# Kernel optimization log

Hardware: AMD Instinct MI355X
Metric: run time of the kernel (lower is better)

## Reference

```python
import jax, jax.numpy as jnp
import numpy as np

K = 8192      # num_embeddings
D = 512       # embedding_dim
DECAY = 0.99
EPS = 1e-5


def setup_inputs() -> dict:
    key = jax.random.key(0)
    k1, k2, k3 = jax.random.split(key, 3)
    inputs = jax.random.normal(k1, (8, 2048, D), dtype=jnp.float32)
    weight = jax.random.normal(k2, (K, D), dtype=jnp.float32) * 0.01
    ema_cluster_size = jnp.ones((K,), dtype=jnp.float32)
    ema_w = jax.random.normal(k3, (K, D), dtype=jnp.float32) * 0.01
    return {"inputs": inputs, "weight": weight,
            "ema_cluster_size": ema_cluster_size, "ema_w": ema_w}


def _l2norm(x):
    return x / jnp.sqrt(jnp.sum(x * x, axis=-1, keepdims=True) + 1e-12)


def reference(inputs, weight, ema_cluster_size, ema_w):
    # Flatten tokens: [N, D]
    flat = inputs.reshape(-1, D)
    cb = _l2norm(weight)            # [K, D]
    xn = _l2norm(flat)              # [N, D]
    # distances = 2 - 2 * sim; argmin(dist) == argmax(sim)
    sim = jnp.einsum('nd,kd->nk', xn, cb)          # [N, K]
    idx = jnp.argmax(sim, axis=1)                  # [N]
    # quantized = one_hot(idx) @ weight  ==  gather
    quantized = weight[idx].reshape(inputs.shape)
    # EMA codebook update (training path)
    counts = jax.ops.segment_sum(jnp.ones_like(idx, dtype=inputs.dtype), idx,
                                 num_segments=K)   # one_hot.sum(0)
    new_cs = ema_cluster_size * DECAY + (1.0 - DECAY) * counts
    n = jnp.sum(new_cs)
    new_cs = (new_cs + EPS) / (n + K * EPS) * n
    dw = jax.ops.segment_sum(flat, idx, num_segments=K)  # one_hot.T @ flat
    new_ema_w = ema_w * DECAY + (1.0 - DECAY) * dw
    new_weight = new_ema_w / new_cs[:, None]
    # Commitment loss and straight-through estimator
    e_latent_loss = jnp.mean((jax.lax.stop_gradient(quantized) - inputs) ** 2)
    quantized_st = inputs + jax.lax.stop_gradient(quantized - inputs)
    return (quantized_st, e_latent_loss, idx[:, None],
            new_cs, new_ema_w, new_weight)
```

## Files before the change

kernel.cpp:

```cpp
#include <hip/hip_runtime.h>
#include <cstdint>
#include <cstddef>

#define NTOK 16384
#define DIM  512
#define KCB  8192
#define MARGIN 6.0e-3f
#define LISTCAP 512

typedef short s16x8 __attribute__((ext_vector_type(8)));
typedef float f32x4 __attribute__((ext_vector_type(4)));

static const size_t WS_XN   = 0;
static const size_t WS_WN   = 16777216;
static const size_t WS_KV   = 25165824;
static const size_t WS_LP   = 37748736;
static const size_t WS_N    = 37847040;
static const size_t WS_CNT  = 37847296;
static const size_t WS_LIST = 37880064;

__device__ __forceinline__ void gl_lds16(const void* g, void* l) {
  __builtin_amdgcn_global_load_lds(
      (__attribute__((address_space(1))) void*)(uintptr_t)g,
      (__attribute__((address_space(3))) void*)(uint32_t)(uintptr_t)l,
      16, 0, 0);
}

__device__ __forceinline__ unsigned short f2bf(float f) {
  unsigned int u = __float_as_uint(f);
  u = (u + 0x7fffu + ((u >> 16) & 1u)) >> 16;
  return (unsigned short)u;
}

__global__ __launch_bounds__(256) void k_normalize(const float* __restrict__ x,
                                                   const float* __restrict__ w,
                                                   unsigned short* __restrict__ xn,
                                                   unsigned short* __restrict__ wn) {
  const int row = blockIdx.x;
  const int tid = threadIdx.x, lane = tid & 63, wave = tid >> 6;
  const float* src;
  unsigned short* dst;
  if (row < NTOK) { src = x + (size_t)row * DIM;          dst = xn + (size_t)row * DIM; }
  else            { src = w + (size_t)(row - NTOK) * DIM; dst = wn + (size_t)(row - NTOK) * DIM; }
  const int e = tid * 2;
  float2 v = *(const float2*)(src + e);
  float ss = v.x * v.x + v.y * v.y;
  #pragma unroll
  for (int off = 32; off > 0; off >>= 1) ss += __shfl_xor(ss, off);
  __shared__ float red[4];
  if (lane == 0) red[wave] = ss;
  __syncthreads();
  const float s = red[0] + red[1] + red[2] + red[3];
  const float inv = rsqrtf(s + 1e-12f);
  unsigned int lo = f2bf(v.x * inv), hi = f2bf(v.y * inv);
  *(unsigned int*)(dst + e) = lo | (hi << 16);
}

__global__ __launch_bounds__(256, 2) void k_gemm_top2(const unsigned short* __restrict__ xn,
                                                      const unsigned short* __restrict__ wn,
                                                      uint2* __restrict__ kv) {
  __shared__ __align__(16) unsigned short smA[128 * 64];
  __shared__ __align__(16) unsigned short smB[256 * 64];
  const int tid = threadIdx.x, wave = tid >> 6, lane = tid & 63;
  const int quad = lane >> 4, col = lane & 15;
  const int wave_m = (wave & 1) * 64, wave_n = (wave >> 1) * 128;
  const int n0 = blockIdx.x * 256, m0 = blockIdx.y * 128;

  const unsigned short* pA[4];
  const unsigned short* pB[8];
  unsigned short* dA[4];
  unsigned short* dB[8];
  #pragma unroll
  for (int i = 0; i < 4; ++i) {
    int s = wave * 256 + i * 64 + lane;
    int row = s >> 3, cg = (s & 7) ^ (row & 7);
    pA[i] = xn + (size_t)(m0 + row) * DIM + cg * 8;
    dA[i] = &smA[(size_t)(wave * 256 + i * 64) * 8];
  }
  #pragma unroll
  for (int i = 0; i < 8; ++i) {
    int s = wave * 512 + i * 64 + lane;
    int row = s >> 3, cg = (s & 7) ^ (row & 7);
    pB[i] = wn + (size_t)(n0 + row) * DIM + cg * 8;
    dB[i] = &smB[(size_t)(wave * 512 + i * 64) * 8];
  }

  int offA[4][2], offB[8][2];
  #pragma unroll
  for (int kbi = 0; kbi < 2; ++kbi) {
    int kb = kbi * 4 + quad;
    #pragma unroll
    for (int mi = 0; mi < 4; ++mi) {
      int row = wave_m + mi * 16 + col;
      offA[mi][kbi] = (row * 8 + (kb ^ (row & 7))) * 16;
    }
    #pragma unroll
    for (int ni = 0; ni < 8; ++ni) {
      int row = wave_n + ni * 16 + col;
      offB[ni][kbi] = (row * 8 + (kb ^ (row & 7))) * 16;
    }
  }

  f32x4 acc[4][8] = {};
  const char* sA = (const char*)smA;
  const char* sB = (const char*)smB;

  #pragma unroll 1
  for (int kt = 0; kt < 8; ++kt) {
    __syncthreads();
    #pragma unroll
    for (int i = 0; i < 4; ++i) { gl_lds16(pA[i], dA[i]); pA[i] += 64; }
    #pragma unroll
    for (int i = 0; i < 8; ++i) { gl_lds16(pB[i], dB[i]); pB[i] += 64; }
    __syncthreads();
    #pragma unroll
    for (int kbi = 0; kbi < 2; ++kbi) {
      s16x8 af[4], bfr[8];
      #pragma unroll
      for (int mi = 0; mi < 4; ++mi) af[mi]  = *(const s16x8*)(sA + offA[mi][kbi]);
      #pragma unroll
      for (int ni = 0; ni < 8; ++ni) bfr[ni] = *(const s16x8*)(sB + offB[ni][kbi]);
      #pragma unroll
      for (int mi = 0; mi < 4; ++mi)
        #pragma unroll
        for (int ni = 0; ni < 8; ++ni)
          acc[mi][ni] = __builtin_amdgcn_mfma_f32_16x16x32_bf16(af[mi], bfr[ni], acc[mi][ni], 0, 0, 0);
    }
  }

  const int tile = blockIdx.x * 2 + (wave >> 1);
  unsigned int rk1 = 0, rk2 = 0;
  #pragma unroll
  for (int mi = 0; mi < 4; ++mi) {
    #pragma unroll
    for (int r = 0; r < 4; ++r) {
      const int p = mi * 4 + r;
      unsigned int k1 = 0, k2 = 0;
      #pragma unroll
      for (int ni = 0; ni < 8; ++ni) {
        float vb = acc[mi][ni][r] + 2.0f;
        unsigned int key = (__float_as_uint(vb) & ~0x7Fu) | (unsigned int)(ni * 16 + col);
        unsigned int mn = min(k1, key);
        k1 = max(k1, key);
        k2 = max(k2, mn);
      }
      #pragma unroll
      for (int off = 1; off < 16; off <<= 1) {
        unsigned int o1 = (unsigned int)__shfl_xor((int)k1, off);
        unsigned int o2 = (unsigned int)__shfl_xor((int)k2, off);
        unsigned int mn = min(k1, o1);
        k1 = max(k1, o1);
        k2 = max(max(k2, o2), mn);
      }
      if (col == p) { rk1 = k1; rk2 = k2; }
    }
  }
  const int row = wave_m + (col >> 2) * 16 + quad * 4 + (col & 3);
  kv[(size_t)(m0 + row) * 64 + tile] = make_uint2(rk1, rk2);
}

__global__ __launch_bounds__(256) void k_select(const float* __restrict__ x,
                                                const float* __restrict__ wgt,
                                                const uint2* __restrict__ kv,
                                                float* __restrict__ out0,
                                                float* __restrict__ out_idx,
                                                float* __restrict__ lp,
                                                int* __restrict__ cnt,
                                                int* __restrict__ list) {
  const int wave = threadIdx.x >> 6, lane = threadIdx.x & 63;
  const int t = blockIdx.x * 4 + wave;

  const uint2 kp = kv[(size_t)t * 64 + lane];
  const float v1 = __uint_as_float(kp.x);
  const float v2 = __uint_as_float(kp.y);
  const int   i1 = lane * 128 + (int)(kp.x & 0x7Fu);

  float gm = v1;
  #pragma unroll
  for (int off = 32; off > 0; off >>= 1) gm = fmaxf(gm, __shfl_xor(gm, off));
  const float thresh = gm - MARGIN;

  unsigned long long m1 = __ballot(v1 >= thresh);
  unsigned long long m2 = __ballot(v2 >= thresh);

  const float* xrow = x + (size_t)t * DIM;
  const float* xr = xrow + lane * 8;
  float4 x0 = *(const float4*)xr;
  float4 x1 = *(const float4*)(xr + 4);
  double xv[8] = {x0.x, x0.y, x0.z, x0.w, x1.x, x1.y, x1.z, x1.w};

  int besti;
  if (__popcll(m1) == 1 && m2 == 0ull) {
    besti = __shfl(i1, __builtin_ctzll(m1));
  } else {
    double bestv = -1e300; besti = 1 << 30;

    auto evalc = [&](int c) {
      const float* wr = wgt + (size_t)c * DIM + lane * 8;
      float4 w0 = *(const float4*)wr;
      float4 w1 = *(const float4*)(wr + 4);
      double s  = (double)w0.x * xv[0] + (double)w0.y * xv[1] + (double)w0.z * xv[2] + (double)w0.w * xv[3]
                + (double)w1.x * xv[4] + (double)w1.y * xv[5] + (double)w1.z * xv[6] + (double)w1.w * xv[7];
      double nw = (double)w0.x * w0.x + (double)w0.y * w0.y + (double)w0.z * w0.z + (double)w0.w * w0.w
                + (double)w1.x * w1.x + (double)w1.y * w1.y + (double)w1.z * w1.z + (double)w1.w * w1.w;
      #pragma unroll
      for (int off = 1; off < 64; off <<= 1) { s += __shfl_xor(s, off); nw += __shfl_xor(nw, off); }
      double sim = s / sqrt(nw + 1e-12);
      if (sim > bestv || (sim == bestv && c < besti)) { bestv = sim; besti = c; }
    };

    unsigned long long w1m = m1;
    while (w1m) {
      int b = __builtin_ctzll(w1m); w1m &= w1m - 1;
      evalc(__shfl(i1, b));
    }
    unsigned long long w2m = m2;
    while (w2m) {
      int b = __builtin_ctzll(w2m); w2m &= w2m - 1;
      #pragma unroll 1
      for (int chunk = 0; chunk < 2; ++chunk) {
        const int c = b * 128 + chunk * 64 + lane;
        const float* wr = wgt + (size_t)c * DIM;
        double s = 0.0, nw = 0.0;
        #pragma unroll 4
        for (int d = 0; d < DIM; d += 4) {
          float4 wv = *(const float4*)(wr + d);
          float4 xw = *(const float4*)(xrow + d);
          s  += (double)wv.x * xw.x + (double)wv.y * xw.y + (double)wv.z * xw.z + (double)wv.w * xw.w;
          nw += (double)wv.x * wv.x + (double)wv.y * wv.y + (double)wv.z * wv.z + (double)wv.w * wv.w;
        }
        double sim = s / sqrt(nw + 1e-12);
        if (sim > bestv || (sim == bestv && c < besti)) { bestv = sim; besti = c; }
      }
    }
    #pragma unroll
    for (int off = 1; off < 64; off <<= 1) {
      double ov = __shfl_xor(bestv, off);
      int    oi = __shfl_xor(besti, off);
      if (ov > bestv || (ov == bestv && oi < besti)) { bestv = ov; besti = oi; }
    }
  }
  if ((unsigned)besti >= KCB) besti = 0;

  const float* wr = wgt + (size_t)besti * DIM + lane * 8;
  float4 w0 = *(const float4*)wr;
  float4 w1 = *(const float4*)(wr + 4);
  float* o0 = out0 + (size_t)t * DIM + lane * 8;
  *(float4*)o0 = w0;
  *(float4*)(o0 + 4) = w1;
  double d2 = 0.0;
  double qv[8] = {w0.x, w0.y, w0.z, w0.w, w1.x, w1.y, w1.z, w1.w};
  #pragma unroll
  for (int j = 0; j < 8; ++j) { double d = qv[j] - xv[j]; d2 += d * d; }
  #pragma unroll
  for (int off = 1; off < 64; off <<= 1) d2 += __shfl_xor(d2, off);

  if (lane == 0) {
    lp[t] = (float)d2;
    out_idx[t] = (float)besti;
    int slot = atomicAdd(&cnt[besti], 1);
    if (slot < LISTCAP) list[besti * LISTCAP + slot] = t;
  }
}

__global__ __launch_bounds__(256) void k_scalars(const float* __restrict__ cs,
                                                 const float* __restrict__ lp,
                                                 double* __restrict__ nacc,
                                                 double* __restrict__ lacc) {
  const int tid = threadIdx.x, b = blockIdx.x;
  const int wave = tid >> 6, lane = tid & 63;
  double s = (double)cs[b * 256 + tid];
  float2 l2 = *(const float2*)(lp + b * 512 + tid * 2);
  double l = (double)l2.x + (double)l2.y;
  #pragma unroll
  for (int off = 32; off > 0; off >>= 1) { s += __shfl_xor(s, off); l += __shfl_xor(l, off); }
  __shared__ double rs[4], rl[4];
  if (lane == 0) { rs[wave] = s; rl[wave] = l; }
  __syncthreads();
  if (tid == 0) {
    atomicAdd(nacc, 0.99 * (rs[0] + rs[1] + rs[2] + rs[3]));
    atomicAdd(lacc, rl[0] + rl[1] + rl[2] + rl[3]);
  }
}

__global__ __launch_bounds__(256) void k_dw(const float* __restrict__ x,
                                            const float* __restrict__ ema_w,
                                            const float* __restrict__ cs,
                                            const int* __restrict__ cnt,
                                            const int* __restrict__ list,
                                            const double* __restrict__ nacc,
                                            const double* __restrict__ lacc,
                                            float* __restrict__ out1,
                                            float* __restrict__ out3,
                                            float* __restrict__ out4,
                                            float* __restrict__ out5) {
  const int c = blockIdx.x, tid = threadIdx.x;
  const int mtrue = cnt[c];
  const int m = mtrue > LISTCAP ? LISTCAP : mtrue;
  const double n = *nacc + 0.01 * (double)NTOK;
  const float prec = cs[c] * 0.99f + 0.01f * (float)mtrue;
  const float csf = (float)(((double)prec + 1e-5) / (n + (double)KCB * 1e-5) * n);
  if (c == 0 && tid == 0) out1[0] = (float)(*lacc / (double)((size_t)NTOK * DIM));
  const int d0 = tid * 2;
  double s0 = 0.0, s1 = 0.0;
  for (int j = 0; j < m; ++j) {
    int t = list[c * LISTCAP + j] & (NTOK - 1);
    float2 v = *(const float2*)(x + (size_t)t * DIM + d0);
    s0 += (double)v.x; s1 += (double)v.y;
  }
  const size_t e = (size_t)c * DIM + d0;
  float n0 = ema_w[e]     * 0.99f + 0.01f * (float)s0;
  float n1 = ema_w[e + 1] * 0.99f + 0.01f * (float)s1;
  out4[e] = n0;       out4[e + 1] = n1;
  out5[e] = n0 / csf; out5[e + 1] = n1 / csf;
  if (tid == 0) out3[c] = csf;
}

extern "C" void kernel_launch(void* const* d_in, const int* in_sizes, int n_in,
                              void* d_out, int out_size, void* d_ws, size_t ws_size,
                              hipStream_t stream) {
  const float* x    = (const float*)d_in[0];
  const float* wgt  = (const float*)d_in[1];
  const float* cs   = (const float*)d_in[2];
  const float* emaw = (const float*)d_in[3];

  char* ws = (char*)d_ws;
  unsigned short* xn  = (unsigned short*)(ws + WS_XN);
  unsigned short* wn  = (unsigned short*)(ws + WS_WN);
  uint2* kv    = (uint2*)(ws + WS_KV);
  float* lp    = (float*)(ws + WS_LP);
  double* nacc = (double*)(ws + WS_N);
  double* lacc = nacc + 1;
  int*   cnt   = (int*)(ws + WS_CNT);
  int*   list  = (int*)(ws + WS_LIST);

  float* out0 = (float*)d_out;
  float* out1 = out0 + 8388608;
  float* out2 = out1 + 1;
  float* out3 = out2 + NTOK;
  float* out4 = out3 + KCB;
  float* out5 = out4 + (size_t)KCB * DIM;

  hipMemsetAsync(cnt, 0, KCB * sizeof(int), stream);
  hipMemsetAsync(ws + WS_N, 0, 2 * sizeof(double), stream);

  k_normalize<<<NTOK + KCB, 256, 0, stream>>>(x, wgt, xn, wn);
  k_gemm_top2<<<dim3(32, 128), 256, 0, stream>>>(xn, wn, kv);
  k_select<<<NTOK / 4, 256, 0, stream>>>(x, wgt, kv, out0, out2, lp, cnt, list);
  k_scalars<<<32, 256, 0, stream>>>(cs, lp, nacc, lacc);
  k_dw<<<KCB, 256, 0, stream>>>(x, emaw, cs, cnt, list, nacc, lacc, out1, out3, out4, out5);
}
```

Baseline: 347.5 us.

## Fold memsets and scalar reduction into normalize and dw kernels; one row per wave

Removes the two hipMemsetAsync calls and the k_scalars launch. The count zeroing and per-wave partial sums of cluster sizes move into k_normalize, which now handles one row per wave with float4 loads and needs no block-level sync. k_dw finishes the cluster-size sum from the partials in every block and computes the loss mean in block 0. This cuts launch count and per-launch overhead, at the cost of a small redundant reduction in each k_dw block and a serial loss loop in block 0.

```diff
diff --git a/kernel.cpp b/kernel.cpp
--- a/kernel.cpp
+++ b/kernel.cpp
@@ -15,7 +15,7 @@
 static const size_t WS_WN   = 16777216;
 static const size_t WS_KV   = 25165824;
 static const size_t WS_LP   = 37748736;
-static const size_t WS_N    = 37847040;
+static const size_t WS_CSP  = 37814272;
 static const size_t WS_CNT  = 37847296;
 static const size_t WS_LIST = 37880064;
 
@@ -26,34 +26,47 @@
       16, 0, 0);
 }
 
-__device__ __forceinline__ unsigned short f2bf(float f) {
+__device__ __forceinline__ unsigned int f2bf(float f) {
   unsigned int u = __float_as_uint(f);
   u = (u + 0x7fffu + ((u >> 16) & 1u)) >> 16;
-  return (unsigned short)u;
+  return u;
 }
 
 __global__ __launch_bounds__(256) void k_normalize(const float* __restrict__ x,
                                                    const float* __restrict__ w,
                                                    unsigned short* __restrict__ xn,
-                                                   unsigned short* __restrict__ wn) {
-  const int row = blockIdx.x;
-  const int tid = threadIdx.x, lane = tid & 63, wave = tid >> 6;
+                                                   unsigned short* __restrict__ wn,
+                                                   const float* __restrict__ cs,
+                                                   double* __restrict__ csp,
+                                                   int* __restrict__ cnt) {
+  const int wave = threadIdx.x >> 6, lane = threadIdx.x & 63;
+  const int row = blockIdx.x * 4 + wave;
   const float* src;
   unsigned short* dst;
   if (row < NTOK) { src = x + (size_t)row * DIM;          dst = xn + (size_t)row * DIM; }
   else            { src = w + (size_t)(row - NTOK) * DIM; dst = wn + (size_t)(row - NTOK) * DIM; }
-  const int e = tid * 2;
-  float2 v = *(const float2*)(src + e);
-  float ss = v.x * v.x + v.y * v.y;
+  const float4 a = *(const float4*)(src + lane * 8);
+  const float4 b = *(const float4*)(src + lane * 8 + 4);
+  float ss = a.x * a.x + a.y * a.y + a.z * a.z + a.w * a.w
+           + b.x * b.x + b.y * b.y + b.z * b.z + b.w * b.w;
   #pragma unroll
   for (int off = 32; off > 0; off >>= 1) ss += __shfl_xor(ss, off);
-  __shared__ float red[4];
-  if (lane == 0) red[wave] = ss;
-  __syncthreads();
-  const float s = red[0] + red[1] + red[2] + red[3];
-  const float inv = rsqrtf(s + 1e-12f);
-  unsigned int lo = f2bf(v.x * inv), hi = f2bf(v.y * inv);
-  *(unsigned int*)(dst + e) = lo | (hi << 16);
+  const float inv = rsqrtf(ss + 1e-12f);
+  uint4 o;
+  o.x = f2bf(a.x * inv) | (f2bf(a.y * inv) << 16);
+  o.y = f2bf(a.z * inv) | (f2bf(a.w * inv) << 16);
+  o.z = f2bf(b.x * inv) | (f2bf(b.y * inv) << 16);
+  o.w = f2bf(b.z * inv) | (f2bf(b.w * inv) << 16);
+  *(uint4*)(dst + lane * 8) = o;
+
+  if (blockIdx.x < 32) {
+    const int i = blockIdx.x * 256 + threadIdx.x;
+    cnt[i] = 0;
+    double s = (double)cs[i];
+    #pragma unroll
+    for (int off = 32; off > 0; off >>= 1) s += __shfl_xor(s, off);
+    if (lane == 0) csp[blockIdx.x * 4 + wave] = s;
+  }
 }
 
 __global__ __launch_bounds__(256, 2) void k_gemm_top2(const unsigned short* __restrict__ xn,
@@ -263,44 +276,33 @@
   }
 }
 
-__global__ __launch_bounds__(256) void k_scalars(const float* __restrict__ cs,
-                                                 const float* __restrict__ lp,
-                                                 double* __restrict__ nacc,
-                                                 double* __restrict__ lacc) {
-  const int tid = threadIdx.x, b = blockIdx.x;
-  const int wave = tid >> 6, lane = tid & 63;
-  double s = (double)cs[b * 256 + tid];
-  float2 l2 = *(const float2*)(lp + b * 512 + tid * 2);
-  double l = (double)l2.x + (double)l2.y;
-  #pragma unroll
-  for (int off = 32; off > 0; off >>= 1) { s += __shfl_xor(s, off); l += __shfl_xor(l, off); }
-  __shared__ double rs[4], rl[4];
-  if (lane == 0) { rs[wave] = s; rl[wave] = l; }
-  __syncthreads();
-  if (tid == 0) {
-    atomicAdd(nacc, 0.99 * (rs[0] + rs[1] + rs[2] + rs[3]));
-    atomicAdd(lacc, rl[0] + rl[1] + rl[2] + rl[3]);
-  }
-}
-
 __global__ __launch_bounds__(256) void k_dw(const float* __restrict__ x,
                                             const float* __restrict__ ema_w,
                                             const float* __restrict__ cs,
                                             const int* __restrict__ cnt,
                                             const int* __restrict__ list,
-                                            const double* __restrict__ nacc,
-                                            const double* __restrict__ lacc,
+                                            const double* __restrict__ csp,
+                                            const float* __restrict__ lp,
                                             float* __restrict__ out1,
                                             float* __restrict__ out3,
                                             float* __restrict__ out4,
                                             float* __restrict__ out5) {
   const int c = blockIdx.x, tid = threadIdx.x;
+  const int wave = tid >> 6, lane = tid & 63;
+  __shared__ double sh_n;
+  if (tid < 64) {
+    double s = csp[tid] + csp[tid + 64];
+    #pragma unroll
+    for (int off = 32; off > 0; off >>= 1) s += __shfl_xor(s, off);
+    if (tid == 0) sh_n = 0.99 * s + 0.01 * (double)NTOK;
+  }
+  __syncthreads();
+  const double n = sh_n;
+
   const int mtrue = cnt[c];
   const int m = mtrue > LISTCAP ? LISTCAP : mtrue;
-  const double n = *nacc + 0.01 * (double)NTOK;
   const float prec = cs[c] * 0.99f + 0.01f * (float)mtrue;
   const float csf = (float)(((double)prec + 1e-5) / (n + (double)KCB * 1e-5) * n);
-  if (c == 0 && tid == 0) out1[0] = (float)(*lacc / (double)((size_t)NTOK * DIM));
   const int d0 = tid * 2;
   double s0 = 0.0, s1 = 0.0;
   for (int j = 0; j < m; ++j) {
@@ -314,6 +316,20 @@
   out4[e] = n0;       out4[e + 1] = n1;
   out5[e] = n0 / csf; out5[e + 1] = n1 / csf;
   if (tid == 0) out3[c] = csf;
+
+  if (c == 0) {
+    double l = 0.0;
+    for (int i = tid * 4; i < NTOK; i += 1024) {
+      float4 l4 = *(const float4*)(lp + i);
+      l += (double)l4.x + (double)l4.y + (double)l4.z + (double)l4.w;
+    }
+    #pragma unroll
+    for (int off = 32; off > 0; off >>= 1) l += __shfl_xor(l, off);
+    __shared__ double rl[4];
+    if (lane == 0) rl[wave] = l;
+    __syncthreads();
+    if (tid == 0) out1[0] = (float)((rl[0] + rl[1] + rl[2] + rl[3]) / (double)((size_t)NTOK * DIM));
+  }
 }
 
 extern "C" void kernel_launch(void* const* d_in, const int* in_sizes, int n_in,
@@ -329,8 +345,7 @@
   unsigned short* wn  = (unsigned short*)(ws + WS_WN);
   uint2* kv    = (uint2*)(ws + WS_KV);
   float* lp    = (float*)(ws + WS_LP);
-  double* nacc = (double*)(ws + WS_N);
-  double* lacc = nacc + 1;
+  double* csp  = (double*)(ws + WS_CSP);
   int*   cnt   = (int*)(ws + WS_CNT);
   int*   list  = (int*)(ws + WS_LIST);
 
@@ -341,12 +356,8 @@
   float* out4 = out3 + KCB;
   float* out5 = out4 + (size_t)KCB * DIM;
 
-  hipMemsetAsync(cnt, 0, KCB * sizeof(int), stream);
-  hipMemsetAsync(ws + WS_N, 0, 2 * sizeof(double), stream);
-
-  k_normalize<<<NTOK + KCB, 256, 0, stream>>>(x, wgt, xn, wn);
+  k_normalize<<<(NTOK + KCB) / 4, 256, 0, stream>>>(x, wgt, xn, wn, cs, csp, cnt);
   k_gemm_top2<<<dim3(32, 128), 256, 0, stream>>>(xn, wn, kv);
   k_select<<<NTOK / 4, 256, 0, stream>>>(x, wgt, kv, out0, out2, lp, cnt, list);
-  k_scalars<<<32, 256, 0, stream>>>(cs, lp, nacc, lacc);
-  k_dw<<<KCB, 256, 0, stream>>>(x, emaw, cs, cnt, list, nacc, lacc, out1, out3, out4, out5);
-}
+  k_dw<<<KCB, 256, 0, stream>>>(x, emaw, cs, cnt, list, csp, lp, out1, out3, out4, out5);
+}
```

New measurement: 342.5 us. Within noise of the previous version (-1.4%).
